# Kernel optimization log

Hardware: AMD Instinct MI355X
Metric: run time of the kernel (lower is better)

The kernel has to match this reference:

```python
import jax, jax.numpy as jnp
import numpy as np

B, S, D, H, T = 512, 256, 64, 256, 50
IN = 2 * D + 1  # LSTM input dim = input_size*2+1
NSUB = 8       # RK4 substeps per output interval
TIME_OFFSET = 0.0

def _xavier(k, shape):
    fan_out, fan_in = shape
    lim = float(np.sqrt(6.0 / (fan_in + fan_out)))
    return jax.random.uniform(k, shape, minval=-lim, maxval=lim, dtype=jnp.float32)

def setup_inputs() -> dict:
    key = jax.random.key(0)
    ks = jax.random.split(key, 12)
    gaps = jax.random.uniform(ks[3], (B, T), minval=0.05, maxval=0.2, dtype=jnp.float32)
    return {
        "x": jax.random.normal(ks[0], (B, S, IN), jnp.float32),
        "lengths": jax.random.randint(ks[1], (B,), S // 2, S + 1),
        "label_feature": jax.random.normal(ks[2], (B, T, D), jnp.float32),
        "label_time": jnp.cumsum(gaps, axis=1),  # sorted per-sample times
        "label_mask": (jax.random.uniform(ks[4], (B, T, D)) < 0.2).astype(jnp.float32),
        "W_ih": _xavier(ks[5], (4 * H, IN)),
        "W_hh": _xavier(ks[6], (4 * H, H)),
        "b_ih": jnp.zeros((4 * H,), jnp.float32),
        "b_hh": jnp.zeros((4 * H,), jnp.float32),
        "Wp1": _xavier(ks[7], (H, H)), "bp1": jnp.zeros((H,), jnp.float32),
        "Wp2": _xavier(ks[8], (D, H)), "bp2": jnp.zeros((D,), jnp.float32),
        "Wd1": _xavier(ks[9], (H, D)), "bd1": jnp.zeros((H,), jnp.float32),
        "Wd2": _xavier(ks[10], (D, H)), "bd2": jnp.zeros((D,), jnp.float32),
    }

def _forward(x, label_feature, label_time, label_mask,
             W_ih, W_hh, b_ih, b_hh, Wp1, bp1, Wp2, bp2, Wd1, bd1, Wd2, bd2,
             lengths):
    # --- LSTM encoder (PyTorch gate order i, f, g, o) ---
    xW = jnp.einsum('bsi,gi->bsg', x, W_ih) + b_ih  # [B,S,4H]
    h0 = jnp.zeros((x.shape[0], H), x.dtype)
    def step(carry, xt):
        h, c = carry
        g = xt + h @ W_hh.T + b_hh
        i, f, gg, o = jnp.split(g, 4, axis=-1)
        c = jax.nn.sigmoid(f) * c + jax.nn.sigmoid(i) * jnp.tanh(gg)
        h = jax.nn.sigmoid(o) * jnp.tanh(c)
        return (h, c), h
    _, hs = jax.lax.scan(step, (h0, h0), jnp.swapaxes(xW, 0, 1))
    hs = jnp.swapaxes(hs, 0, 1)  # [B,S,H]
    # masked mean over valid timesteps
    mask = (jnp.arange(x.shape[1])[None, :] < lengths[:, None]).astype(x.dtype)
    pooled = (hs * mask[:, :, None]).sum(axis=1) / lengths[:, None].astype(x.dtype)
    # projection MLP -> initial ODE state
    y0 = jax.nn.relu(pooled @ Wp1.T + bp1) @ Wp2.T + bp2  # [B,D]
    # --- batched Neural-ODE integration (fixed-step RK4) ---
    def deriv(y):
        return jax.nn.relu(y @ Wd1.T + bd1) @ Wd2.T + bd2
    ts = label_time - TIME_OFFSET
    dts = (ts[:, 1:] - ts[:, :-1]) / NSUB  # [B,T-1]
    def interval(y, dt_b):
        dt = dt_b[:, None]
        for _ in range(NSUB):
            k1 = deriv(y)
            k2 = deriv(y + 0.5 * dt * k1)
            k3 = deriv(y + 0.5 * dt * k2)
            k4 = deriv(y + dt * k3)
            y = y + (dt / 6.0) * (k1 + 2.0 * k2 + 2.0 * k3 + k4)
        return y, y
    _, traj = jax.lax.scan(interval, y0, jnp.swapaxes(dts, 0, 1))  # [T-1,B,D]
    predict = jnp.swapaxes(jnp.concatenate([y0[None], traj], axis=0), 0, 1)  # [B,T,D]
    loss = (predict - label_feature) ** 2 * (1.0 - label_mask)
    return predict, loss

def reference(x, lengths, label_feature, label_time, label_mask,
              W_ih, W_hh, b_ih, b_hh, Wp1, bp1, Wp2, bp2, Wd1, bd1, Wd2, bd2):
    return _forward(x, label_feature, label_time, label_mask,
                    W_ih, W_hh, b_ih, b_hh, Wp1, bp1, Wp2, bp2, Wd1, bd1, Wd2, bd2,
                    lengths)
```

## Files before the change

### kernel.cpp

```cpp
#include <hip/hip_runtime.h>
#include <hip/hip_bf16.h>

#define BB 512
#define SS 256
#define HH 256
#define DD 64
#define TT 50
#define GG 1024
#define INW 129

typedef _Float16 h4 __attribute__((ext_vector_type(4)));
typedef _Float16 h8 __attribute__((ext_vector_type(8)));
typedef __fp16 hf2 __attribute__((ext_vector_type(2)));
typedef float f32x4 __attribute__((ext_vector_type(4)));
typedef unsigned int u32;

__device__ inline float sigf(float x) { return 1.f / (1.f + __expf(-x)); }
__device__ inline float tanhf_(float x) { return 1.f - 2.f / (__expf(2.f * x) + 1.f); }

__device__ inline u32 pkrtz(float a, float b) {
    hf2 h = __builtin_amdgcn_cvt_pkrtz(a, b);
    return __builtin_bit_cast(u32, h);
}

__global__ __launch_bounds__(256) void prep_kernel(
    const float* __restrict__ W_hh, const float* __restrict__ W_ih,
    const float* __restrict__ Wd1, const float* __restrict__ Wd2,
    h4* __restrict__ BhhV4, h4* __restrict__ BhhL4, h4* __restrict__ BhhS4,
    _Float16* __restrict__ Bih, h4* __restrict__ A1f4, h4* __restrict__ A2f4)
{
    int idx = blockIdx.x * 256 + threadIdx.x;
    if (idx < 65536) {
        int eh = idx & 1;
        int l = (idx >> 1) & 63;
        int ks = (idx >> 7) & 7;
        int s = (idx >> 10) & 7;
        int w = (idx >> 13) & 7;
        int g = s & 3, jt = s >> 2;
        int n = g * 256 + w * 32 + jt * 16 + (l & 15);
        int k = 32 * ks + 8 * (l >> 4) + 4 * eh;
        float4 v = *(const float4*)(W_hh + (size_t)n * HH + k);
        h4 o; o[0] = (_Float16)v.x; o[1] = (_Float16)v.y; o[2] = (_Float16)v.z; o[3] = (_Float16)v.w;
        if (ks < 3)
            BhhV4[(((w * 8 + s) * 3 + ks) * 64 + l) * 2 + eh] = o;
        else if (ks == 4 || ks == 5)
            BhhL4[(((w * 8 + s) * 2 + (ks - 4)) * 64 + l) * 2 + eh] = o;
        else {
            int sub = (ks == 6) ? 0 : (ks == 7) ? 1 : 2;
            BhhS4[(((w * 8 + s) * 3 + sub) * 64 + l) * 2 + eh] = o;
        }
    } else if (idx < 106496) {
        int fj = idx - 65536;
        int eh = fj & 1;
        int l = (fj >> 1) & 63;
        int si = fj >> 7;
        int ks = si % 5;
        int ntile = si / 5;
        int n = ntile * 16 + (l & 15);
        int k = 32 * ks + 8 * (l >> 4) + 4 * eh;
        h4 o;
#pragma unroll
        for (int i = 0; i < 4; i++) {
            int kk = k + i;
            o[i] = (_Float16)((kk < INW) ? W_ih[(size_t)n * INW + kk] : 0.f);
        }
        *(h4*)(Bih + (size_t)fj * 4) = o;
    } else if (idx < 110592) {
        int fj = idx - 106496;
        int eh = fj & 1;
        int l = (fj >> 1) & 63;
        int slot = fj >> 7;
        int ks = slot & 1, t = slot >> 1;
        int row = 16 * t + (l & 15);
        int k = 32 * ks + 8 * (l >> 4) + 4 * eh;
        h4 o;
#pragma unroll
        for (int i = 0; i < 4; i++) o[i] = (_Float16)Wd1[(size_t)row * DD + k + i];
        A1f4[fj] = o;
    } else if (idx < 114688) {
        int fj = idx - 110592;
        int eh = fj & 1;
        int l = (fj >> 1) & 63;
        int slot = fj >> 7;
        int ks = slot & 7, t2 = slot >> 3;
        int row = 16 * t2 + (l & 15);
        int k = 32 * ks + 8 * (l >> 4) + 4 * eh;
        h4 o;
#pragma unroll
        for (int i = 0; i < 4; i++) o[i] = (_Float16)Wd2[(size_t)row * HH + k + i];
        A2f4[fj] = o;
    }
}

__global__ __launch_bounds__(256) void xw_kernel(
    const float* __restrict__ x, const _Float16* __restrict__ Bih,
    const float* __restrict__ b_ih, const float* __restrict__ b_hh,
    h4* __restrict__ xwf)
{
    __shared__ __align__(16) _Float16 ash[4][5][64][8];
    int tid = threadIdx.x;
    int w4 = tid >> 6, l = tid & 63;
    int bx = blockIdx.x;
    int t = bx >> 3, Bb = bx & 7;

    for (int i = tid; i < 64 * 160; i += 256) {
        int rr = i / 160, kk = i % 160;
        float v = (kk < INW) ? x[((size_t)(Bb * 64 + rr) * SS + t) * INW + kk] : 0.f;
        ash[rr >> 4][kk >> 5][(((kk & 31) >> 3) << 4) + (rr & 15)][kk & 7] = (_Float16)v;
    }
    __syncthreads();

    h8 A[4][5];
#pragma unroll
    for (int ms = 0; ms < 4; ms++)
#pragma unroll
        for (int ks = 0; ks < 5; ks++)
            A[ms][ks] = *(h8*)&ash[ms][ks][l][0];

    const h8* Bih8 = (const h8*)Bih;
    for (int nt16 = 0; nt16 < 16; nt16++) {
        int ntile = w4 * 16 + nt16;
        h8 Bv[5];
#pragma unroll
        for (int ks = 0; ks < 5; ks++) Bv[ks] = Bih8[(ntile * 5 + ks) * 64 + l];
        int nb = ntile * 16 + (l & 15);
        float bias = b_ih[nb] + b_hh[nb];
        f32x4 acc[4];
#pragma unroll
        for (int ms = 0; ms < 4; ms++) acc[ms] = (f32x4){0.f, 0.f, 0.f, 0.f};
#pragma unroll
        for (int ks = 0; ks < 5; ks++)
#pragma unroll
            for (int ms = 0; ms < 4; ms++)
                acc[ms] = __builtin_amdgcn_mfma_f32_16x16x32_f16(A[ms][ks], Bv[ks], acc[ms], 0, 0, 0);
        int slot = ((ntile & 15) >> 1) * 8 + (ntile & 1) * 4 + (ntile >> 4);
#pragma unroll
        for (int ms = 0; ms < 4; ms++) {
            int bg = Bb * 4 + ms;
            h4 o;
#pragma unroll
            for (int r = 0; r < 4; r++) o[r] = (_Float16)(acc[ms][r] + bias);
            xwf[(((size_t)bg * SS + t) * 64 + slot) * 64 + l] = o;
        }
    }
}

__global__ __launch_bounds__(512, 2) void lstm_kernel(
    const h8* __restrict__ BhhV, const h8* __restrict__ BhhL, const h8* __restrict__ BhhS,
    const h4* __restrict__ xwf, const int* __restrict__ lengths, float* __restrict__ pooled)
{
    __shared__ __align__(16) _Float16 Wlds[65536];
    __shared__ __align__(16) _Float16 hbuf[2][8][64][8];
    int tid = threadIdx.x;
    int w = tid >> 6, l = tid & 63;
    int bg = blockIdx.x;

    {
        const uint4* src = (const uint4*)BhhL;
        uint4* dst = (uint4*)Wlds;
#pragma unroll
        for (int i = 0; i < 16; i++) dst[i * 512 + tid] = src[i * 512 + tid];
    }

    h8 Wv[8][3];
#pragma unroll
    for (int s = 0; s < 8; s++)
#pragma unroll
        for (int ks = 0; ks < 3; ks++)
            Wv[s][ks] = BhhV[((w * 8 + s) * 3 + ks) * 64 + l];

    int len_[4];
    float c_[2][4], pa[2][4];
#pragma unroll
    for (int r = 0; r < 4; r++) {
        int b = 4 * (l >> 4) + r;
        len_[r] = lengths[bg * 16 + b];
#pragma unroll
        for (int jt = 0; jt < 2; jt++) { c_[jt][r] = 0.f; pa[jt][r] = 0.f; }
    }

    {
        uint4* hz = (uint4*)hbuf;
        hz[tid] = make_uint4(0, 0, 0, 0);
        hz[512 + tid] = make_uint4(0, 0, 0, 0);
    }
    __syncthreads();

    h4 xc[8], xn[8];
    {
        const h4* p0 = xwf + (((size_t)bg * SS + 0) * 64 + w * 8) * 64 + l;
#pragma unroll
        for (int s = 0; s < 8; s++) xc[s] = p0[s * 64];
    }

    int cur = 0;
    for (int t = 0; t < SS; t++) {
        int tn = (t + 1) & 255;
        const h4* pn = xwf + (((size_t)bg * SS + tn) * 64 + w * 8) * 64 + l;
#pragma unroll
        for (int s = 0; s < 8; s++) xn[s] = pn[s * 64];

        int zoff = 0;
        asm volatile("" : "+v"(zoff));
        const h8* bS = BhhS + zoff;
#pragma unroll
        for (int jt = 0; jt < 2; jt++) {
            h8 Ws6[4], Ws7[4], Ws3[4];
#pragma unroll
            for (int g = 0; g < 4; g++) {
                Ws6[g] = bS[((w * 8 + jt * 4 + g) * 3 + 0) * 64 + l];
                Ws7[g] = bS[((w * 8 + jt * 4 + g) * 3 + 1) * 64 + l];
            }
            f32x4 acc[4];
#pragma unroll
            for (int g = 0; g < 4; g++) acc[g] = (f32x4){0.f, 0.f, 0.f, 0.f};
#pragma unroll
            for (int ks = 0; ks < 3; ks++) {
                h8 A = *(const h8*)&hbuf[cur][ks][l][0];
#pragma unroll
                for (int g = 0; g < 4; g++)
                    acc[g] = __builtin_amdgcn_mfma_f32_16x16x32_f16(A, Wv[jt * 4 + g][ks], acc[g], 0, 0, 0);
            }
            {
                h8 A = *(const h8*)&hbuf[cur][6][l][0];
#pragma unroll
                for (int g = 0; g < 4; g++)
                    acc[g] = __builtin_amdgcn_mfma_f32_16x16x32_f16(A, Ws6[g], acc[g], 0, 0, 0);
            }
#pragma unroll
            for (int g = 0; g < 4; g++) Ws3[g] = bS[((w * 8 + jt * 4 + g) * 3 + 2) * 64 + l];
#pragma unroll
            for (int ks = 4; ks < 6; ks++) {
                h8 A = *(const h8*)&hbuf[cur][ks][l][0];
#pragma unroll
                for (int g = 0; g < 4; g++) {
                    h8 Bw = *(const h8*)&Wlds[(((w * 8 + jt * 4 + g) * 2 + (ks - 4)) * 64 + l) * 8];
                    acc[g] = __builtin_amdgcn_mfma_f32_16x16x32_f16(A, Bw, acc[g], 0, 0, 0);
                }
            }
            {
                h8 A = *(const h8*)&hbuf[cur][7][l][0];
#pragma unroll
                for (int g = 0; g < 4; g++)
                    acc[g] = __builtin_amdgcn_mfma_f32_16x16x32_f16(A, Ws7[g], acc[g], 0, 0, 0);
            }
            {
                h8 A = *(const h8*)&hbuf[cur][3][l][0];
#pragma unroll
                for (int g = 0; g < 4; g++)
                    acc[g] = __builtin_amdgcn_mfma_f32_16x16x32_f16(A, Ws3[g], acc[g], 0, 0, 0);
            }
#pragma unroll
            for (int r = 0; r < 4; r++) {
                float gi = acc[0][r] + (float)xc[jt * 4 + 0][r];
                float gf = acc[1][r] + (float)xc[jt * 4 + 1][r];
                float gg = acc[2][r] + (float)xc[jt * 4 + 2][r];
                float go = acc[3][r] + (float)xc[jt * 4 + 3][r];
                float cc = sigf(gf) * c_[jt][r] + sigf(gi) * tanhf_(gg);
                c_[jt][r] = cc;
                float hh = sigf(go) * tanhf_(cc);
                if (t < len_[r]) pa[jt][r] += hh;
                int b = 4 * (l >> 4) + r;
                int j = w * 32 + jt * 16 + (l & 15);
                hbuf[cur ^ 1][j >> 5][(((j & 31) >> 3) << 4) + b][j & 7] = (_Float16)hh;
            }
        }
        __syncthreads();
#pragma unroll
        for (int s = 0; s < 8; s++) xc[s] = xn[s];
        cur ^= 1;
    }

#pragma unroll
    for (int jt = 0; jt < 2; jt++)
#pragma unroll
        for (int r = 0; r < 4; r++) {
            int b = 4 * (l >> 4) + r;
            int j = w * 32 + jt * 16 + (l & 15);
            pooled[(size_t)(bg * 16 + b) * HH + j] = pa[jt][r] / (float)len_[r];
        }
}

__global__ __launch_bounds__(256) void head_kernel(
    const float* __restrict__ pooled, const float* __restrict__ Wp1,
    const float* __restrict__ bp1, const float* __restrict__ Wp2,
    const float* __restrict__ bp2, float* __restrict__ y0ws)
{
    __shared__ __align__(16) float psh[HH];
    __shared__ __align__(16) float rsh[HH];
    int tid = threadIdx.x, b = blockIdx.x;
    psh[tid] = pooled[(size_t)b * HH + tid];
    __syncthreads();
    float a = bp1[tid];
    const float* wr = Wp1 + (size_t)tid * HH;
#pragma unroll 8
    for (int k = 0; k < HH; k += 4) {
        float4 w = *(const float4*)(wr + k);
        a += psh[k] * w.x + psh[k + 1] * w.y + psh[k + 2] * w.z + psh[k + 3] * w.w;
    }
    rsh[tid] = fmaxf(a, 0.f);
    __syncthreads();
    if (tid < DD) {
        float acc = bp2[tid];
        const float* w2 = Wp2 + (size_t)tid * HH;
#pragma unroll 8
        for (int h = 0; h < HH; h += 4) {
            float4 w = *(const float4*)(w2 + h);
            acc += rsh[h] * w.x + rsh[h + 1] * w.y + rsh[h + 2] * w.z + rsh[h + 3] * w.w;
        }
        y0ws[(size_t)b * DD + tid] = acc;
    }
}

__global__ __launch_bounds__(256) void ode_kernel(
    const float* __restrict__ y0ws, const h8* __restrict__ A1f,
    const float* __restrict__ bd1, const h8* __restrict__ A2f,
    const float* __restrict__ bd2, const float* __restrict__ ltime,
    const float* __restrict__ lfeat, const float* __restrict__ lmask,
    float* __restrict__ pred, float* __restrict__ losso)
{
    __shared__ __align__(16) _Float16 hX[16 * 264];
    __shared__ __align__(16) _Float16 kX[16 * 80];
    int tid = threadIdx.x;
    int wv = tid >> 6, l = tid & 63;
    int q = l >> 4, bb = l & 15;
    int b = blockIdx.x * 16 + bb;

    h8 A1[4][2];
#pragma unroll
    for (int tt = 0; tt < 4; tt++)
#pragma unroll
        for (int ks = 0; ks < 2; ks++)
            A1[tt][ks] = A1f[((4 * wv + tt) * 2 + ks) * 64 + l];
    h8 A2[8];
#pragma unroll
    for (int ks = 0; ks < 8; ks++) A2[ks] = A2f[(wv * 8 + ks) * 64 + l];

    f32x4 BD1[4];
#pragma unroll
    for (int tt = 0; tt < 4; tt++)
#pragma unroll
        for (int r = 0; r < 4; r++) BD1[tt][r] = bd1[16 * (4 * wv + tt) + 4 * q + r];
    f32x4 BD2;
#pragma unroll
    for (int r = 0; r < 4; r++) BD2[r] = bd2[16 * wv + 4 * q + r];

    float y[16], kp[16], ksum[16];
#pragma unroll
    for (int ks2 = 0; ks2 < 2; ks2++)
#pragma unroll
        for (int e = 0; e < 8; e++) {
            y[ks2 * 8 + e] = y0ws[(size_t)b * DD + 32 * ks2 + 8 * q + e];
            kp[ks2 * 8 + e] = 0.f;
        }

    if (wv == 0) {
#pragma unroll
        for (int ks2 = 0; ks2 < 2; ks2++) {
            size_t idx = ((size_t)b * TT + 0) * DD + 32 * ks2 + 8 * q;
#pragma unroll
            for (int h4i = 0; h4i < 2; h4i++) {
                float4 p;
                p.x = y[ks2 * 8 + 4 * h4i + 0]; p.y = y[ks2 * 8 + 4 * h4i + 1];
                p.z = y[ks2 * 8 + 4 * h4i + 2]; p.w = y[ks2 * 8 + 4 * h4i + 3];
                *(float4*)&pred[idx + 4 * h4i] = p;
                float4 lf = *(const float4*)&lfeat[idx + 4 * h4i];
                float4 lm = *(const float4*)&lmask[idx + 4 * h4i];
                float4 lo;
                lo.x = (p.x - lf.x) * (p.x - lf.x) * (1.f - lm.x);
                lo.y = (p.y - lf.y) * (p.y - lf.y) * (1.f - lm.y);
                lo.z = (p.z - lf.z) * (p.z - lf.z) * (1.f - lm.z);
                lo.w = (p.w - lf.w) * (p.w - lf.w) * (1.f - lm.w);
                *(float4*)&losso[idx + 4 * h4i] = lo;
            }
        }
    }

    for (int iv = 0; iv < TT - 1; iv++) {
        float t0 = ltime[(size_t)b * TT + iv], t1 = ltime[(size_t)b * TT + iv + 1];
        float dt = (t1 - t0) * 0.125f;
        for (int ss = 0; ss < 8; ss++) {
#pragma unroll
            for (int i = 0; i < 16; i++) ksum[i] = 0.f;
            const float AE[4] = {0.f, 0.5f, 0.5f, 1.f};
            const float WE[4] = {1.f, 2.f, 2.f, 1.f};
#pragma unroll
            for (int e = 0; e < 4; e++) {
                float adt = AE[e] * dt;
                h8 B1[2];
#pragma unroll
                for (int ks2 = 0; ks2 < 2; ks2++) {
                    uint4 u;
                    u.x = pkrtz(y[ks2 * 8 + 0] + adt * kp[ks2 * 8 + 0], y[ks2 * 8 + 1] + adt * kp[ks2 * 8 + 1]);
                    u.y = pkrtz(y[ks2 * 8 + 2] + adt * kp[ks2 * 8 + 2], y[ks2 * 8 + 3] + adt * kp[ks2 * 8 + 3]);
                    u.z = pkrtz(y[ks2 * 8 + 4] + adt * kp[ks2 * 8 + 4], y[ks2 * 8 + 5] + adt * kp[ks2 * 8 + 5]);
                    u.w = pkrtz(y[ks2 * 8 + 6] + adt * kp[ks2 * 8 + 6], y[ks2 * 8 + 7] + adt * kp[ks2 * 8 + 7]);
                    B1[ks2] = __builtin_bit_cast(h8, u);
                }
                f32x4 C1[4];
#pragma unroll
                for (int tt = 0; tt < 4; tt++) C1[tt] = BD1[tt];
#pragma unroll
                for (int ks2 = 0; ks2 < 2; ks2++)
#pragma unroll
                    for (int tt = 0; tt < 4; tt++)
                        C1[tt] = __builtin_amdgcn_mfma_f32_16x16x32_f16(A1[tt][ks2], B1[ks2], C1[tt], 0, 0, 0);
#pragma unroll
                for (int tt = 0; tt < 4; tt++) {
                    u32 p0 = pkrtz(fmaxf(C1[tt][0], 0.f), fmaxf(C1[tt][1], 0.f));
                    u32 p1 = pkrtz(fmaxf(C1[tt][2], 0.f), fmaxf(C1[tt][3], 0.f));
                    *(uint2*)&hX[bb * 264 + 16 * (4 * wv + tt) + 4 * q] = make_uint2(p0, p1);
                }
                __syncthreads();
                f32x4 Ca = BD2, Cb = (f32x4){0.f, 0.f, 0.f, 0.f};
#pragma unroll
                for (int ksi = 0; ksi < 8; ksi += 2) {
                    h8 B2a = *(const h8*)&hX[bb * 264 + 32 * ksi + 8 * q];
                    h8 B2b = *(const h8*)&hX[bb * 264 + 32 * (ksi + 1) + 8 * q];
                    Ca = __builtin_amdgcn_mfma_f32_16x16x32_f16(A2[ksi], B2a, Ca, 0, 0, 0);
                    Cb = __builtin_amdgcn_mfma_f32_16x16x32_f16(A2[ksi + 1], B2b, Cb, 0, 0, 0);
                }
                {
                    u32 p0 = pkrtz(Ca[0] + Cb[0], Ca[1] + Cb[1]);
                    u32 p1 = pkrtz(Ca[2] + Cb[2], Ca[3] + Cb[3]);
                    *(uint2*)&kX[bb * 80 + 16 * wv + 4 * q] = make_uint2(p0, p1);
                }
                __syncthreads();
#pragma unroll
                for (int ks2 = 0; ks2 < 2; ks2++) {
                    h8 kf = *(const h8*)&kX[bb * 80 + 32 * ks2 + 8 * q];
#pragma unroll
                    for (int e2 = 0; e2 < 8; e2++) {
                        float kv = (float)kf[e2];
                        kp[ks2 * 8 + e2] = kv;
                        ksum[ks2 * 8 + e2] += WE[e] * kv;
                    }
                }
            }
#pragma unroll
            for (int i = 0; i < 16; i++) y[i] += dt * (1.f / 6.f) * ksum[i];
        }
        if (wv == 0) {
#pragma unroll
            for (int ks2 = 0; ks2 < 2; ks2++) {
                size_t idx = ((size_t)b * TT + iv + 1) * DD + 32 * ks2 + 8 * q;
#pragma unroll
                for (int h4i = 0; h4i < 2; h4i++) {
                    float4 p;
                    p.x = y[ks2 * 8 + 4 * h4i + 0]; p.y = y[ks2 * 8 + 4 * h4i + 1];
                    p.z = y[ks2 * 8 + 4 * h4i + 2]; p.w = y[ks2 * 8 + 4 * h4i + 3];
                    *(float4*)&pred[idx + 4 * h4i] = p;
                    float4 lf = *(const float4*)&lfeat[idx + 4 * h4i];
                    float4 lm = *(const float4*)&lmask[idx + 4 * h4i];
                    float4 lo;
                    lo.x = (p.x - lf.x) * (p.x - lf.x) * (1.f - lm.x);
                    lo.y = (p.y - lf.y) * (p.y - lf.y) * (1.f - lm.y);
                    lo.z = (p.z - lf.z) * (p.z - lf.z) * (1.f - lm.z);
                    lo.w = (p.w - lf.w) * (p.w - lf.w) * (1.f - lm.w);
                    *(float4*)&losso[idx + 4 * h4i] = lo;
                }
            }
        }
    }
}

extern "C" void kernel_launch(void* const* d_in, const int* in_sizes, int n_in,
                              void* d_out, int out_size, void* d_ws, size_t ws_size,
                              hipStream_t stream)
{
    const float* x      = (const float*)d_in[0];
    const int* lengths  = (const int*)d_in[1];
    const float* lfeat  = (const float*)d_in[2];
    const float* ltime  = (const float*)d_in[3];
    const float* lmask  = (const float*)d_in[4];
    const float* W_ih   = (const float*)d_in[5];
    const float* W_hh   = (const float*)d_in[6];
    const float* b_ih   = (const float*)d_in[7];
    const float* b_hh   = (const float*)d_in[8];
    const float* Wp1    = (const float*)d_in[9];
    const float* bp1    = (const float*)d_in[10];
    const float* Wp2    = (const float*)d_in[11];
    const float* bp2    = (const float*)d_in[12];
    const float* Wd1    = (const float*)d_in[13];
    const float* bd1    = (const float*)d_in[14];
    const float* Wd2    = (const float*)d_in[15];
    const float* bd2    = (const float*)d_in[16];

    float* pred  = (float*)d_out;
    float* losso = pred + (size_t)BB * TT * DD;

    char* ws = (char*)d_ws;
    h4*       xwf    = (h4*)(ws + 0);
    h4*       BhhV   = (h4*)(ws + 268435456);
    h4*       BhhL   = (h4*)(ws + 268632064);
    h4*       BhhS   = (h4*)(ws + 268763136);
    _Float16* Bih    = (_Float16*)(ws + 268959744);
    float*    pooled = (float*)(ws + 269287424);
    float*    y0ws   = (float*)(ws + 269811712);
    h4*       A1f    = (h4*)(ws + 269942784);
    h4*       A2f    = (h4*)(ws + 269975552);

    prep_kernel<<<448, 256, 0, stream>>>(W_hh, W_ih, Wd1, Wd2, BhhV, BhhL, BhhS, Bih, A1f, A2f);
    xw_kernel<<<2048, 256, 0, stream>>>(x, Bih, b_ih, b_hh, xwf);
    lstm_kernel<<<32, 512, 0, stream>>>((const h8*)BhhV, (const h8*)BhhL, (const h8*)BhhS,
                                        xwf, lengths, pooled);
    head_kernel<<<BB, 256, 0, stream>>>(pooled, Wp1, bp1, Wp2, bp2, y0ws);
    ode_kernel<<<32, 256, 0, stream>>>(y0ws, (const h8*)A1f, bd1, (const h8*)A2f, bd2,
                                       ltime, lfeat, lmask, pred, losso);
}
```

Before: 2.582 ms.

## Rebalance LSTM weight split between registers and streamed loads; pack ODE groups per block

```diff
diff --git a/kernel.cpp b/kernel.cpp
--- a/kernel.cpp
+++ b/kernel.cpp
@@ -41,14 +41,9 @@
         int k = 32 * ks + 8 * (l >> 4) + 4 * eh;
         float4 v = *(const float4*)(W_hh + (size_t)n * HH + k);
         h4 o; o[0] = (_Float16)v.x; o[1] = (_Float16)v.y; o[2] = (_Float16)v.z; o[3] = (_Float16)v.w;
-        if (ks < 3)
-            BhhV4[(((w * 8 + s) * 3 + ks) * 64 + l) * 2 + eh] = o;
-        else if (ks == 4 || ks == 5)
-            BhhL4[(((w * 8 + s) * 2 + (ks - 4)) * 64 + l) * 2 + eh] = o;
-        else {
-            int sub = (ks == 6) ? 0 : (ks == 7) ? 1 : 2;
-            BhhS4[(((w * 8 + s) * 3 + sub) * 64 + l) * 2 + eh] = o;
-        }
+        if (ks < 4)      BhhV4[(((w * 8 + s) * 4 + ks) * 64 + l) * 2 + eh] = o;
+        else if (ks < 6) BhhL4[(((w * 8 + s) * 2 + (ks - 4)) * 64 + l) * 2 + eh] = o;
+        else             BhhS4[(((w * 8 + s) * 2 + (ks - 6)) * 64 + l) * 2 + eh] = o;
     } else if (idx < 106496) {
         int fj = idx - 65536;
         int eh = fj & 1;
@@ -162,12 +157,12 @@
         for (int i = 0; i < 16; i++) dst[i * 512 + tid] = src[i * 512 + tid];
     }
 
-    h8 Wv[8][3];
+    h8 Wv[8][4];
 #pragma unroll
     for (int s = 0; s < 8; s++)
 #pragma unroll
-        for (int ks = 0; ks < 3; ks++)
-            Wv[s][ks] = BhhV[((w * 8 + s) * 3 + ks) * 64 + l];
+        for (int ks = 0; ks < 4; ks++)
+            Wv[s][ks] = BhhV[((w * 8 + s) * 4 + ks) * 64 + l];
 
     int len_[4];
     float c_[2][4], pa[2][4];
@@ -186,36 +181,25 @@
     }
     __syncthreads();
 
-    h4 xc[8], xn[8];
-    {
-        const h4* p0 = xwf + (((size_t)bg * SS + 0) * 64 + w * 8) * 64 + l;
-#pragma unroll
-        for (int s = 0; s < 8; s++) xc[s] = p0[s * 64];
-    }
-
     int cur = 0;
     for (int t = 0; t < SS; t++) {
-        int tn = (t + 1) & 255;
-        const h4* pn = xwf + (((size_t)bg * SS + tn) * 64 + w * 8) * 64 + l;
-#pragma unroll
-        for (int s = 0; s < 8; s++) xn[s] = pn[s * 64];
-
+        const h4* xpb = xwf + (((size_t)bg * SS + t) * 64 + w * 8) * 64 + l;
         int zoff = 0;
         asm volatile("" : "+v"(zoff));
         const h8* bS = BhhS + zoff;
 #pragma unroll
         for (int jt = 0; jt < 2; jt++) {
-            h8 Ws6[4], Ws7[4], Ws3[4];
-#pragma unroll
-            for (int g = 0; g < 4; g++) {
-                Ws6[g] = bS[((w * 8 + jt * 4 + g) * 3 + 0) * 64 + l];
-                Ws7[g] = bS[((w * 8 + jt * 4 + g) * 3 + 1) * 64 + l];
-            }
+            h4 xv[4];
+#pragma unroll
+            for (int g = 0; g < 4; g++) xv[g] = xpb[(jt * 4 + g) * 64];
+            h8 Ws[4];
+#pragma unroll
+            for (int g = 0; g < 4; g++) Ws[g] = bS[((w * 8 + jt * 4 + g) * 2 + 0) * 64 + l];
             f32x4 acc[4];
 #pragma unroll
             for (int g = 0; g < 4; g++) acc[g] = (f32x4){0.f, 0.f, 0.f, 0.f};
 #pragma unroll
-            for (int ks = 0; ks < 3; ks++) {
+            for (int ks = 0; ks < 4; ks++) {
                 h8 A = *(const h8*)&hbuf[cur][ks][l][0];
 #pragma unroll
                 for (int g = 0; g < 4; g++)
@@ -225,10 +209,10 @@
                 h8 A = *(const h8*)&hbuf[cur][6][l][0];
 #pragma unroll
                 for (int g = 0; g < 4; g++)
-                    acc[g] = __builtin_amdgcn_mfma_f32_16x16x32_f16(A, Ws6[g], acc[g], 0, 0, 0);
-            }
-#pragma unroll
-            for (int g = 0; g < 4; g++) Ws3[g] = bS[((w * 8 + jt * 4 + g) * 3 + 2) * 64 + l];
+                    acc[g] = __builtin_amdgcn_mfma_f32_16x16x32_f16(A, Ws[g], acc[g], 0, 0, 0);
+            }
+#pragma unroll
+            for (int g = 0; g < 4; g++) Ws[g] = bS[((w * 8 + jt * 4 + g) * 2 + 1) * 64 + l];
 #pragma unroll
             for (int ks = 4; ks < 6; ks++) {
                 h8 A = *(const h8*)&hbuf[cur][ks][l][0];
@@ -242,20 +226,14 @@
                 h8 A = *(const h8*)&hbuf[cur][7][l][0];
 #pragma unroll
                 for (int g = 0; g < 4; g++)
-                    acc[g] = __builtin_amdgcn_mfma_f32_16x16x32_f16(A, Ws7[g], acc[g], 0, 0, 0);
-            }
-            {
-                h8 A = *(const h8*)&hbuf[cur][3][l][0];
-#pragma unroll
-                for (int g = 0; g < 4; g++)
-                    acc[g] = __builtin_amdgcn_mfma_f32_16x16x32_f16(A, Ws3[g], acc[g], 0, 0, 0);
+                    acc[g] = __builtin_amdgcn_mfma_f32_16x16x32_f16(A, Ws[g], acc[g], 0, 0, 0);
             }
 #pragma unroll
             for (int r = 0; r < 4; r++) {
-                float gi = acc[0][r] + (float)xc[jt * 4 + 0][r];
-                float gf = acc[1][r] + (float)xc[jt * 4 + 1][r];
-                float gg = acc[2][r] + (float)xc[jt * 4 + 2][r];
-                float go = acc[3][r] + (float)xc[jt * 4 + 3][r];
+                float gi = acc[0][r] + (float)xv[0][r];
+                float gf = acc[1][r] + (float)xv[1][r];
+                float gg = acc[2][r] + (float)xv[2][r];
+                float go = acc[3][r] + (float)xv[3][r];
                 float cc = sigf(gf) * c_[jt][r] + sigf(gi) * tanhf_(gg);
                 c_[jt][r] = cc;
                 float hh = sigf(go) * tanhf_(cc);
@@ -266,8 +244,6 @@
             }
         }
         __syncthreads();
-#pragma unroll
-        for (int s = 0; s < 8; s++) xc[s] = xn[s];
         cur ^= 1;
     }
 
@@ -312,19 +288,23 @@
     }
 }
 
-__global__ __launch_bounds__(256) void ode_kernel(
+__global__ __launch_bounds__(1024, 4) void ode_kernel(
     const float* __restrict__ y0ws, const h8* __restrict__ A1f,
     const float* __restrict__ bd1, const h8* __restrict__ A2f,
     const float* __restrict__ bd2, const float* __restrict__ ltime,
     const float* __restrict__ lfeat, const float* __restrict__ lmask,
     float* __restrict__ pred, float* __restrict__ losso)
 {
-    __shared__ __align__(16) _Float16 hX[16 * 264];
-    __shared__ __align__(16) _Float16 kX[16 * 80];
+    __shared__ __align__(16) _Float16 hX[4][16 * 264];
+    __shared__ __align__(16) _Float16 kX[4][16 * 80];
     int tid = threadIdx.x;
-    int wv = tid >> 6, l = tid & 63;
+    int grp = tid >> 8;
+    int t256 = tid & 255;
+    int wv = t256 >> 6, l = t256 & 63;
     int q = l >> 4, bb = l & 15;
-    int b = blockIdx.x * 16 + bb;
+    int b = (blockIdx.x * 4 + grp) * 16 + bb;
+    _Float16* hXg = hX[grp];
+    _Float16* kXg = kX[grp];
 
     h8 A1[4][2];
 #pragma unroll
@@ -409,26 +389,26 @@
                 for (int tt = 0; tt < 4; tt++) {
                     u32 p0 = pkrtz(fmaxf(C1[tt][0], 0.f), fmaxf(C1[tt][1], 0.f));
                     u32 p1 = pkrtz(fmaxf(C1[tt][2], 0.f), fmaxf(C1[tt][3], 0.f));
-                    *(uint2*)&hX[bb * 264 + 16 * (4 * wv + tt) + 4 * q] = make_uint2(p0, p1);
+                    *(uint2*)&hXg[bb * 264 + 16 * (4 * wv + tt) + 4 * q] = make_uint2(p0, p1);
                 }
                 __syncthreads();
                 f32x4 Ca = BD2, Cb = (f32x4){0.f, 0.f, 0.f, 0.f};
 #pragma unroll
                 for (int ksi = 0; ksi < 8; ksi += 2) {
-                    h8 B2a = *(const h8*)&hX[bb * 264 + 32 * ksi + 8 * q];
-                    h8 B2b = *(const h8*)&hX[bb * 264 + 32 * (ksi + 1) + 8 * q];
+                    h8 B2a = *(const h8*)&hXg[bb * 264 + 32 * ksi + 8 * q];
+                    h8 B2b = *(const h8*)&hXg[bb * 264 + 32 * (ksi + 1) + 8 * q];
                     Ca = __builtin_amdgcn_mfma_f32_16x16x32_f16(A2[ksi], B2a, Ca, 0, 0, 0);
                     Cb = __builtin_amdgcn_mfma_f32_16x16x32_f16(A2[ksi + 1], B2b, Cb, 0, 0, 0);
                 }
                 {
                     u32 p0 = pkrtz(Ca[0] + Cb[0], Ca[1] + Cb[1]);
                     u32 p1 = pkrtz(Ca[2] + Cb[2], Ca[3] + Cb[3]);
-                    *(uint2*)&kX[bb * 80 + 16 * wv + 4 * q] = make_uint2(p0, p1);
+                    *(uint2*)&kXg[bb * 80 + 16 * wv + 4 * q] = make_uint2(p0, p1);
                 }
                 __syncthreads();
 #pragma unroll
                 for (int ks2 = 0; ks2 < 2; ks2++) {
-                    h8 kf = *(const h8*)&kX[bb * 80 + 32 * ks2 + 8 * q];
+                    h8 kf = *(const h8*)&kXg[bb * 80 + 32 * ks2 + 8 * q];
 #pragma unroll
                     for (int e2 = 0; e2 < 8; e2++) {
                         float kv = (float)kf[e2];
@@ -492,8 +472,8 @@
     char* ws = (char*)d_ws;
     h4*       xwf    = (h4*)(ws + 0);
     h4*       BhhV   = (h4*)(ws + 268435456);
-    h4*       BhhL   = (h4*)(ws + 268632064);
-    h4*       BhhS   = (h4*)(ws + 268763136);
+    h4*       BhhL   = (h4*)(ws + 268697600);
+    h4*       BhhS   = (h4*)(ws + 268828672);
     _Float16* Bih    = (_Float16*)(ws + 268959744);
     float*    pooled = (float*)(ws + 269287424);
     float*    y0ws   = (float*)(ws + 269811712);
@@ -505,6 +485,6 @@
     lstm_kernel<<<32, 512, 0, stream>>>((const h8*)BhhV, (const h8*)BhhL, (const h8*)BhhS,
                                         xwf, lengths, pooled);
     head_kernel<<<BB, 256, 0, stream>>>(pooled, Wp1, bp1, Wp2, bp2, y0ws);
-    ode_kernel<<<32, 256, 0, stream>>>(y0ws, (const h8*)A1f, bd1, (const h8*)A2f, bd2,
+    ode_kernel<<<8, 1024, 0, stream>>>(y0ws, (const h8*)A1f, bd1, (const h8*)A2f, bd2,
                                        ltime, lfeat, lmask, pred, losso);
 }
```

New measurement: 9.372 ms. +263.0%, slower.
